# Kernel optimization log

Measured on AMD Instinct MI355X. Metric: run time of the kernel, lower is better.

Reference implementation:

```python
import jax, jax.numpy as jnp
import numpy as np

B, C, H, W_, N, E = 8, 256, 128, 128, 4096, 128
EPS = 1e-12  # torch F.normalize default eps


def grid_sample_points(x, kpts):
    """Bilinear grid_sample at point coords, padding_mode='zeros', align_corners=False.
    x: [B,C,H,W], kpts: [B,N,2] in [-1,1] (x,y order) -> [B,C,N].
    """
    Bx, Cx, Hx, Wx = x.shape
    # unnormalize (align_corners=False)
    ix = (kpts[..., 0] + 1.0) * (Wx * 0.5) - 0.5  # [B,N]
    iy = (kpts[..., 1] + 1.0) * (Hx * 0.5) - 0.5
    x0f = jnp.floor(ix)
    y0f = jnp.floor(iy)
    wx = ix - x0f  # fractional weights
    wy = iy - y0f
    x0 = x0f.astype(jnp.int32)
    y0 = y0f.astype(jnp.int32)
    x1 = x0 + 1
    y1 = y0 + 1

    def gather(xi, yi):
        valid = (xi >= 0) & (xi < Wx) & (yi >= 0) & (yi < Hx)  # [B,N]
        xc = jnp.clip(xi, 0, Wx - 1)
        yc = jnp.clip(yi, 0, Hx - 1)
        # per-batch gather of [C] vectors at N points -> [B,C,N]
        v = jax.vmap(lambda xb, yy, xx: xb[:, yy, xx])(x, yc, xc)
        return v * valid[:, None, :].astype(x.dtype)

    v00 = gather(x0, y0)
    v10 = gather(x1, y0)
    v01 = gather(x0, y1)
    v11 = gather(x1, y1)
    wxb = wx[:, None, :]
    wyb = wy[:, None, :]
    return (v00 * (1 - wxb) * (1 - wyb)
            + v10 * wxb * (1 - wyb)
            + v01 * (1 - wxb) * wyb
            + v11 * wxb * wyb)


def setup_inputs() -> dict:
    key = jax.random.key(0)
    k1, k2, k3 = jax.random.split(key, 3)
    x = jax.random.normal(k1, (B, C, H, W_), dtype=jnp.float32)
    # keypoints in normalized [-1,1] coords (grid_sample convention)
    kpts = jax.random.uniform(k2, (B, N, 2), dtype=jnp.float32) * 2.0 - 1.0
    # xavier_normal_(gain=0.1) for Linear(C -> E)
    std = 0.1 * np.sqrt(2.0 / (C + E))
    whiten_w = jax.random.normal(k3, (E, C), dtype=jnp.float32) * std
    whiten_b = jnp.zeros((E,), dtype=jnp.float32)
    return {"x": x, "kpts": kpts, "whiten_w": whiten_w, "whiten_b": whiten_b}


def reference(x, kpts, whiten_w, whiten_b):
    desc = grid_sample_points(x, kpts)              # [B,C,N]
    desc = jnp.transpose(desc, (0, 2, 1))           # [B,N,C]
    desc = jnp.einsum('bnc,ec->bne', desc, whiten_w) + whiten_b  # [B,N,E]
    norm = jnp.maximum(jnp.linalg.norm(desc, axis=2, keepdims=True), EPS)
    return desc / norm
```

## Files before the change

kernel.cpp:

```cpp
#include <hip/hip_runtime.h>
#include <hip/hip_bf16.h>
#include <math.h>

#define BB 8
#define CC 256
#define HH 128
#define WW 128
#define NN 4096
#define EE 128

typedef __bf16 bf16x8 __attribute__((ext_vector_type(8)));
typedef __bf16 bf16x4 __attribute__((ext_vector_type(4)));
typedef float f32x4 __attribute__((ext_vector_type(4)));

#define WF_OFF    0
#define DESCF_OFF 65536
#define WS_NEED   (65536ull + 16777216ull)

__device__ __forceinline__ void async_copy16(const float* g, float* l) {
  __builtin_amdgcn_global_load_lds(
      (const __attribute__((address_space(1))) void*)g,
      (__attribute__((address_space(3))) void*)l, 16, 0, 0);
}

__global__ __launch_bounds__(512, 4) void gather_kernel(
    const float* __restrict__ x, const float* __restrict__ kpts,
    const float* __restrict__ W, __bf16* __restrict__ descf,
    __bf16* __restrict__ Wf) {
  __shared__ float plane[HH * WW];
  int blk = blockIdx.x;
  int b = blk >> 6, g = blk & 63;
  int t = threadIdx.x;
  int w = t >> 6, lane = t & 63;
  const float* xg = x + ((size_t)((b << 8) + (g << 2)) << 14);
  {
    const float* gs = xg + w * 2048 + lane * 4;
    float* ls = plane + w * 2048;
#pragma unroll
    for (int i = 0; i < 8; ++i) async_copy16(gs + i * 256, ls + i * 256);
  }
  if (blk < 256 && t < 128) {
    int i = (blk << 7) + t;
    int j = i & 7, ln = (i >> 3) & 63, etile = (i >> 9) & 7, kstep = (i >> 12) & 7;
    Wf[i] = (__bf16)W[(etile * 16 + (ln & 15)) * CC + kstep * 32 + ((ln >> 4) << 3) + j];
  }
  int base[8];
  float4 wt[8];
  const float2* kp = (const float2*)(kpts + ((size_t)(b * NN) << 1));
#pragma unroll
  for (int i = 0; i < 8; ++i) {
    int n = t + (i << 9);
    float2 k2 = kp[n];
    float ix = (k2.x + 1.f) * (WW * 0.5f) - 0.5f;
    float iy = (k2.y + 1.f) * (HH * 0.5f) - 0.5f;
    float x0f = floorf(ix), y0f = floorf(iy);
    float wx = ix - x0f, wy = iy - y0f;
    int x0 = (int)x0f, y0 = (int)y0f;
    float ax0 = (x0 >= 0 && x0 < WW) ? (1.f - wx) : 0.f;
    float ax1 = (x0 + 1 >= 0 && x0 + 1 < WW) ? wx : 0.f;
    float ay0 = (y0 >= 0 && y0 < HH) ? (1.f - wy) : 0.f;
    float ay1 = (y0 + 1 >= 0 && y0 + 1 < HH) ? wy : 0.f;
    int bx = min(max(x0, 0), WW - 2);
    int by = min(max(y0, 0), HH - 2);
    float a0 = 0.f, a1 = 0.f, c0 = 0.f, c1 = 0.f;
    if (x0 == bx) a0 += ax0; else if (x0 == bx + 1) a1 += ax0;
    if (x0 + 1 == bx) a0 += ax1; else if (x0 + 1 == bx + 1) a1 += ax1;
    if (y0 == by) c0 += ay0; else if (y0 == by + 1) c1 += ay0;
    if (y0 + 1 == by) c0 += ay1; else if (y0 + 1 == by + 1) c1 += ay1;
    base[i] = by * WW + bx;
    wt[i] = make_float4(a0 * c0, a1 * c0, a0 * c1, a1 * c1);
  }
  bf16x4 res[8];
#pragma unroll
  for (int p = 0; p < 4; ++p) {
    __syncthreads();
#pragma unroll
    for (int i = 0; i < 8; ++i) {
      int bs = base[i];
      float4 ww = wt[i];
      float v = plane[bs] * ww.x + plane[bs + 1] * ww.y
              + plane[bs + WW] * ww.z + plane[bs + WW + 1] * ww.w;
      res[i][p] = (__bf16)v;
    }
    __syncthreads();
    if (p < 3) {
      const float* gs = xg + (p + 1) * 16384 + w * 2048 + lane * 4;
      float* ls = plane + w * 2048;
#pragma unroll
      for (int i = 0; i < 8; ++i) async_copy16(gs + i * 256, ls + i * 256);
    }
  }
  int c0i = g << 2;
  int kstep = c0i >> 5, quad = (c0i >> 3) & 3, j0 = c0i & 7;
#pragma unroll
  for (int i = 0; i < 8; ++i) {
    int n = t + (i << 9);
    size_t off = (((size_t)((b << 8) + (n >> 4))) << 12)
               + ((size_t)kstep << 9) + ((size_t)quad << 7) + ((size_t)(n & 15) << 3) + j0;
    *(bf16x4*)(descf + off) = res[i];
  }
}

__global__ __launch_bounds__(256) void gemm_norm_kernel(
    const __bf16* __restrict__ descf, const __bf16* __restrict__ Wf,
    const float* __restrict__ bias, float* __restrict__ out) {
  __shared__ __bf16 wlds[8 * 8 * 64 * 8];
  int t = threadIdx.x;
  {
    const float4* src = (const float4*)Wf;
    float4* d = (float4*)wlds;
#pragma unroll
    for (int i = 0; i < 16; ++i) d[t + 256 * i] = src[t + 256 * i];
  }
  __syncthreads();
  int blk = blockIdx.x;
  int b = blk >> 6;
  int wave = t >> 6, lane = t & 63;
  int ntile = ((blk & 63) << 2) + wave;
  const bf16x8* bsrc =
      (const bf16x8*)(descf + ((size_t)b << 20) + ((size_t)ntile << 12));
  bf16x8 bfrag[8];
#pragma unroll
  for (int k = 0; k < 8; ++k) bfrag[k] = bsrc[k * 64 + lane];
  const bf16x8* alds = (const bf16x8*)wlds;
  f32x4 acc[8];
#pragma unroll
  for (int e = 0; e < 8; ++e) acc[e] = (f32x4)(0.f);
#pragma unroll
  for (int k = 0; k < 8; ++k) {
#pragma unroll
    for (int e = 0; e < 8; ++e) {
      bf16x8 a = alds[(k * 8 + e) * 64 + lane];
      acc[e] = __builtin_amdgcn_mfma_f32_16x16x32_bf16(a, bfrag[k], acc[e], 0, 0, 0);
    }
  }
  int quad = lane >> 4, col = lane & 15;
  int n = ntile * 16 + col;
  float s = 0.f;
  float4 av[8];
#pragma unroll
  for (int e = 0; e < 8; ++e) {
    float4 bi = *(const float4*)(bias + e * 16 + quad * 4);
    float4 v = make_float4(acc[e][0] + bi.x, acc[e][1] + bi.y,
                           acc[e][2] + bi.z, acc[e][3] + bi.w);
    av[e] = v;
    s += v.x * v.x + v.y * v.y + v.z * v.z + v.w * v.w;
  }
  s += __shfl_xor(s, 16);
  s += __shfl_xor(s, 32);
  float inv = 1.f / fmaxf(sqrtf(s), 1e-12f);
  float4* out4 = (float4*)out + (((size_t)(b * NN + n)) << 5) + quad;
#pragma unroll
  for (int e = 0; e < 8; ++e)
    out4[e * 4] = make_float4(av[e].x * inv, av[e].y * inv,
                              av[e].z * inv, av[e].w * inv);
}

__global__ __launch_bounds__(128) void fused_fallback(
    const float* __restrict__ x, const float* __restrict__ kpts,
    const float* __restrict__ W, const float* __restrict__ bias,
    float* __restrict__ out) {
  __shared__ float dsc[CC];
  __shared__ float sred[2];
  int blk = blockIdx.x;
  int b = blk >> 12;
  float kx = kpts[2 * blk], ky = kpts[2 * blk + 1];
  float ix = (kx + 1.f) * (WW * 0.5f) - 0.5f;
  float iy = (ky + 1.f) * (HH * 0.5f) - 0.5f;
  float x0f = floorf(ix), y0f = floorf(iy);
  float wx = ix - x0f, wy = iy - y0f;
  int x0 = (int)x0f, y0 = (int)y0f;
  float ax0 = (x0 >= 0 && x0 < WW) ? (1.f - wx) : 0.f;
  float ax1 = (x0 + 1 >= 0 && x0 + 1 < WW) ? wx : 0.f;
  float ay0 = (y0 >= 0 && y0 < HH) ? (1.f - wy) : 0.f;
  float ay1 = (y0 + 1 >= 0 && y0 + 1 < HH) ? wy : 0.f;
  int bx = min(max(x0, 0), WW - 2);
  int by = min(max(y0, 0), HH - 2);
  float a0 = 0.f, a1 = 0.f, r0 = 0.f, r1 = 0.f;
  if (x0 == bx) a0 += ax0; else if (x0 == bx + 1) a1 += ax0;
  if (x0 + 1 == bx) a0 += ax1; else if (x0 + 1 == bx + 1) a1 += ax1;
  if (y0 == by) r0 += ay0; else if (y0 == by + 1) r1 += ay0;
  if (y0 + 1 == by) r0 += ay1; else if (y0 + 1 == by + 1) r1 += ay1;
  int base = by * WW + bx;
  float w00 = a0 * r0, w10 = a1 * r0, w01 = a0 * r1, w11 = a1 * r1;
  int t = threadIdx.x;
  const float* src = x + ((size_t)b << 22);
  for (int c = t; c < CC; c += 128) {
    const float* p = src + ((size_t)c << 14);
    dsc[c] = p[base] * w00 + p[base + 1] * w10 + p[base + WW] * w01 + p[base + WW + 1] * w11;
  }
  __syncthreads();
  float acc = bias[t];
  const float* wr = W + t * CC;
  for (int c = 0; c < CC; ++c) acc += wr[c] * dsc[c];
  float s = acc * acc;
  for (int m = 1; m < 64; m <<= 1) s += __shfl_xor(s, m);
  if ((t & 63) == 0) sred[t >> 6] = s;
  __syncthreads();
  float tot = sred[0] + sred[1];
  float inv = 1.f / fmaxf(sqrtf(tot), 1e-12f);
  out[((size_t)blk << 7) + t] = acc * inv;
}

extern "C" void kernel_launch(void* const* d_in, const int* in_sizes, int n_in,
                              void* d_out, int out_size, void* d_ws, size_t ws_size,
                              hipStream_t stream) {
  const float* x    = (const float*)d_in[0];
  const float* kpts = (const float*)d_in[1];
  const float* W    = (const float*)d_in[2];
  const float* bias = (const float*)d_in[3];
  float* out = (float*)d_out;
  if (ws_size >= WS_NEED) {
    char* ws = (char*)d_ws;
    __bf16* Wf    = (__bf16*)(ws + WF_OFF);
    __bf16* descf = (__bf16*)(ws + DESCF_OFF);
    gather_kernel<<<BB * 64, 512, 0, stream>>>(x, kpts, W, descf, Wf);
    gemm_norm_kernel<<<BB * (NN / 64), 256, 0, stream>>>(descf, Wf, bias, out);
  } else {
    fused_fallback<<<BB * NN, 128, 0, stream>>>(x, kpts, W, bias, out);
  }
}
```

Before: 210.2 us.

## Double-buffer gather planes, 8 channels per block, coalesce output via LDS

The gather kernel now processes 8 channels per block with two LDS plane buffers, prefetching the next plane while the current one is sampled. This hides the global load latency behind compute and allows 16-byte descriptor stores. The grid is halved to 256 blocks and LDS use doubles to 128KB, so occupancy and parallelism drop. The GEMM epilogue stages normalized outputs through LDS so each row is written contiguously instead of in strided float4 stores.

```diff
diff --git a/kernel.cpp b/kernel.cpp
--- a/kernel.cpp
+++ b/kernel.cpp
@@ -10,7 +10,6 @@
 #define EE 128
 
 typedef __bf16 bf16x8 __attribute__((ext_vector_type(8)));
-typedef __bf16 bf16x4 __attribute__((ext_vector_type(4)));
 typedef float f32x4 __attribute__((ext_vector_type(4)));
 
 #define WF_OFF    0
@@ -23,23 +22,23 @@
       (__attribute__((address_space(3))) void*)l, 16, 0, 0);
 }
 
-__global__ __launch_bounds__(512, 4) void gather_kernel(
+__global__ __launch_bounds__(512) void gather_kernel(
     const float* __restrict__ x, const float* __restrict__ kpts,
     const float* __restrict__ W, __bf16* __restrict__ descf,
     __bf16* __restrict__ Wf) {
-  __shared__ float plane[HH * WW];
+  __shared__ float buf[2][HH * WW];
   int blk = blockIdx.x;
-  int b = blk >> 6, g = blk & 63;
+  int b = blk >> 5, g = blk & 31;
   int t = threadIdx.x;
   int w = t >> 6, lane = t & 63;
-  const float* xg = x + ((size_t)((b << 8) + (g << 2)) << 14);
+  const float* xg = x + ((size_t)((b << 8) + (g << 3)) << 14);
   {
     const float* gs = xg + w * 2048 + lane * 4;
-    float* ls = plane + w * 2048;
+    float* ls = buf[0] + w * 2048;
 #pragma unroll
     for (int i = 0; i < 8; ++i) async_copy16(gs + i * 256, ls + i * 256);
   }
-  if (blk < 256 && t < 128) {
+  if (t < 128) {
     int i = (blk << 7) + t;
     int j = i & 7, ln = (i >> 3) & 63, etile = (i >> 9) & 7, kstep = (i >> 12) & 7;
     Wf[i] = (__bf16)W[(etile * 16 + (ln & 15)) * CC + kstep * 32 + ((ln >> 4) << 3) + j];
@@ -70,34 +69,33 @@
     base[i] = by * WW + bx;
     wt[i] = make_float4(a0 * c0, a1 * c0, a0 * c1, a1 * c1);
   }
-  bf16x4 res[8];
-#pragma unroll
-  for (int p = 0; p < 4; ++p) {
+  bf16x8 res[8];
+#pragma unroll
+  for (int p = 0; p < 8; ++p) {
     __syncthreads();
+    if (p < 7) {
+      const float* gs = xg + (p + 1) * 16384 + w * 2048 + lane * 4;
+      float* ls = buf[(p + 1) & 1] + w * 2048;
+#pragma unroll
+      for (int i = 0; i < 8; ++i) async_copy16(gs + i * 256, ls + i * 256);
+    }
+    const float* bcur = buf[p & 1];
 #pragma unroll
     for (int i = 0; i < 8; ++i) {
       int bs = base[i];
       float4 ww = wt[i];
-      float v = plane[bs] * ww.x + plane[bs + 1] * ww.y
-              + plane[bs + WW] * ww.z + plane[bs + WW + 1] * ww.w;
+      float v = bcur[bs] * ww.x + bcur[bs + 1] * ww.y
+              + bcur[bs + WW] * ww.z + bcur[bs + WW + 1] * ww.w;
       res[i][p] = (__bf16)v;
     }
-    __syncthreads();
-    if (p < 3) {
-      const float* gs = xg + (p + 1) * 16384 + w * 2048 + lane * 4;
-      float* ls = plane + w * 2048;
-#pragma unroll
-      for (int i = 0; i < 8; ++i) async_copy16(gs + i * 256, ls + i * 256);
-    }
-  }
-  int c0i = g << 2;
-  int kstep = c0i >> 5, quad = (c0i >> 3) & 3, j0 = c0i & 7;
+  }
+  int kstep = g >> 2, quad = g & 3;
 #pragma unroll
   for (int i = 0; i < 8; ++i) {
     int n = t + (i << 9);
     size_t off = (((size_t)((b << 8) + (n >> 4))) << 12)
-               + ((size_t)kstep << 9) + ((size_t)quad << 7) + ((size_t)(n & 15) << 3) + j0;
-    *(bf16x4*)(descf + off) = res[i];
+               + ((size_t)kstep << 9) + ((size_t)quad << 7) + ((size_t)(n & 15) << 3);
+    *(bf16x8*)(descf + off) = res[i];
   }
 }
 
@@ -135,7 +133,6 @@
     }
   }
   int quad = lane >> 4, col = lane & 15;
-  int n = ntile * 16 + col;
   float s = 0.f;
   float4 av[8];
 #pragma unroll
@@ -149,11 +146,21 @@
   s += __shfl_xor(s, 16);
   s += __shfl_xor(s, 32);
   float inv = 1.f / fmaxf(sqrtf(s), 1e-12f);
-  float4* out4 = (float4*)out + (((size_t)(b * NN + n)) << 5) + quad;
+  __syncthreads();
+  float4* sc = (float4*)wlds;
+  int sbase = wave * 528 + col * 33 + quad;
 #pragma unroll
   for (int e = 0; e < 8; ++e)
-    out4[e * 4] = make_float4(av[e].x * inv, av[e].y * inv,
-                              av[e].z * inv, av[e].w * inv);
+    sc[sbase + e * 4] = make_float4(av[e].x * inv, av[e].y * inv,
+                                    av[e].z * inv, av[e].w * inv);
+  __syncthreads();
+  int e4 = lane & 31, dn = lane >> 5;
+  float4* ob = (float4*)out + (((size_t)(b * NN + ntile * 16)) << 5);
+#pragma unroll
+  for (int i = 0; i < 8; ++i) {
+    int nn = 2 * i + dn;
+    ob[((size_t)nn << 5) + e4] = sc[wave * 528 + nn * 33 + e4];
+  }
 }
 
 __global__ __launch_bounds__(128) void fused_fallback(
@@ -214,7 +221,7 @@
     char* ws = (char*)d_ws;
     __bf16* Wf    = (__bf16*)(ws + WF_OFF);
     __bf16* descf = (__bf16*)(ws + DESCF_OFF);
-    gather_kernel<<<BB * 64, 512, 0, stream>>>(x, kpts, W, descf, Wf);
+    gather_kernel<<<BB * 32, 512, 0, stream>>>(x, kpts, W, descf, Wf);
     gemm_norm_kernel<<<BB * (NN / 64), 256, 0, stream>>>(descf, Wf, bias, out);
   } else {
     fused_fallback<<<BB * NN, 128, 0, stream>>>(x, kpts, W, bias, out);
```

Measured after the change: 210.1 us. About the same (-0.1%).
